# Performance work log

Hardware: AMD Instinct MI355X
Metric: run time of the kernel (lower is better)

Reference implementation:

```python
import jax, jax.numpy as jnp
import numpy as np

B, T, D, KQ, K, V, L = 4, 4096, 256, 32, 4, 8, 4
LN_EPS = 1e-5


def _layernorm(h, g, b):
    mu = h.mean(-1, keepdims=True)
    var = ((h - mu) ** 2).mean(-1, keepdims=True)
    return (h - mu) * jax.lax.rsqrt(var + LN_EPS) * g + b


def _forward(x, attention_mask, Wq, bq, Wk, bk, Wg, bg, W1f, b1f, W2f, b2f,
             ln_g, ln_b, Whh, b_ih, b_hh, Wp, bp, opW1, opb1, opW2, opb2, Wo, bo):
    # ---- DemandRouter ----
    q = x @ Wq + bq                      # [B,T,KQ]
    k = x @ Wk + bk                      # [B,T,KQ]
    sim = jnp.einsum('btk,bsk->bts', q, k) / jnp.sqrt(jnp.float32(KQ))  # [B,T,T]
    mask2 = attention_mask[:, None, :] * attention_mask[:, :, None]
    sim = jnp.where(mask2 == 0, jnp.float32(-1e9), sim)
    gates = jax.nn.sigmoid(x @ Wg + bg)[..., 0]   # [B,T]
    sim = sim * gates[:, :, None]
    _, idx = jax.lax.top_k(sim, K)                # [B,T,K]
    gathered = jax.vmap(lambda xb, ib: xb[ib])(x, idx)  # [B,T,K,D]
    routed_mean = gathered.mean(axis=2)           # [B,T,D]
    # ---- System1Block ----
    ffn = jax.nn.gelu(routed_mean @ W1f + b1f, approximate=False) @ W2f + b2f
    h = _layernorm(routed_mean + ffn, ln_g, ln_b)  # [B,T,D]
    # ---- ProgramGenerator (GRU over zero inputs, h0 = mean-pooled context) ----
    hs = h.mean(axis=1)                           # [B,D]
    outs = []
    for _ in range(L):
        gh = hs @ Whh.T + b_hh                    # [B,3D]
        r = jax.nn.sigmoid(b_ih[:D] + gh[:, :D])
        z = jax.nn.sigmoid(b_ih[D:2 * D] + gh[:, D:2 * D])
        n = jnp.tanh(b_ih[2 * D:] + r * gh[:, 2 * D:])
        hs = (1 - z) * n + z * hs
        outs.append(hs)
    rnn_out = jnp.stack(outs, axis=1)             # [B,L,D]
    program_logits = rnn_out @ Wp + bp            # [B,L,V]
    # ---- NeuralOpLibrary: op outputs are identical across L, so compute once
    # on [B,T,D] and average softmax weights over L (same math as expand+mean).
    op_hidden = jax.nn.relu(jnp.einsum('btd,vde->btve', h, opW1) + opb1)
    op_out = jnp.einsum('btve,ved->btvd', op_hidden, opW2) + opb2  # [B,T,V,D]
    w = jax.nn.softmax(program_logits, axis=-1).mean(axis=1)       # [B,V]
    fused = jnp.einsum('bv,btvd->btd', w, op_out)                   # [B,T,D]
    # ---- pool + output projection ----
    pooled = fused.max(axis=1)                    # [B,D]
    return pooled @ Wo + bo


def setup_inputs() -> dict:
    key = jax.random.key(0)
    ks = jax.random.split(key, 20)
    s = 0.02
    p = lambda i, shape: jax.random.normal(ks[i], shape, jnp.float32) * s
    return {
        'x': jax.random.normal(ks[0], (B, T, D), jnp.float32),
        'attention_mask': jnp.ones((B, T), jnp.float32),
        'Wq': p(1, (D, KQ)), 'bq': jnp.zeros((KQ,), jnp.float32),
        'Wk': p(2, (D, KQ)), 'bk': jnp.zeros((KQ,), jnp.float32),
        'Wg': p(3, (D, 1)), 'bg': jnp.zeros((1,), jnp.float32),
        'W1f': p(4, (D, 2 * D)), 'b1f': jnp.zeros((2 * D,), jnp.float32),
        'W2f': p(5, (2 * D, D)), 'b2f': jnp.zeros((D,), jnp.float32),
        'ln_g': jnp.ones((D,), jnp.float32), 'ln_b': jnp.zeros((D,), jnp.float32),
        'Whh': p(6, (3 * D, D)), 'b_ih': p(7, (3 * D,)), 'b_hh': p(8, (3 * D,)),
        'Wp': p(9, (D, V)), 'bp': jnp.zeros((V,), jnp.float32),
        'opW1': p(10, (V, D, D)), 'opb1': jnp.zeros((V, D), jnp.float32),
        'opW2': p(11, (V, D, D)), 'opb2': jnp.zeros((V, D), jnp.float32),
        'Wo': p(12, (D, D)), 'bo': jnp.zeros((D,), jnp.float32),
    }


def reference(x, attention_mask, Wq, bq, Wk, bk, Wg, bg, W1f, b1f, W2f, b2f,
              ln_g, ln_b, Whh, b_ih, b_hh, Wp, bp, opW1, opb1, opW2, opb2, Wo, bo):
    return _forward(x, attention_mask, Wq, bq, Wk, bk, Wg, bg, W1f, b1f, W2f, b2f,
                    ln_g, ln_b, Whh, b_ih, b_hh, Wp, bp, opW1, opb1, opW2, opb2, Wo, bo)
```

## Files before the change

### kernel.cpp

```cpp
#include <hip/hip_runtime.h>

#define BB 4
#define TT 4096
#define DD 256
#define KQ 32
#define TOPK 4
#define NV 8
#define NL 4
#define MROWS (BB*TT)
#define NSC 8
#define SSPAN 512
#define NCAND (NSC*16)

typedef __attribute__((ext_vector_type(8))) __bf16 bf16x8;
typedef __attribute__((ext_vector_type(4))) float  f32x4;

__device__ __forceinline__ unsigned short f2bf(float f) {
  union { float f; unsigned u; } un; un.f = f;
  unsigned r = un.u + 0x7fffu + ((un.u >> 16) & 1u);
  return (unsigned short)(r >> 16);
}
__device__ __forceinline__ float b2f(unsigned short s) {
  union { unsigned u; float f; } un; un.u = ((unsigned)s) << 16;
  return un.f;
}

__device__ __forceinline__ void ins4(float val, int s, float v[4], int id[4]) {
  if (val <= v[3]) return;
  v[3] = val; id[3] = s;
  #pragma unroll
  for (int j = 3; j > 0; --j) {
    if (v[j] > v[j-1]) {
      float tv = v[j]; v[j] = v[j-1]; v[j-1] = tv;
      int   ti = id[j]; id[j] = id[j-1]; id[j-1] = ti;
    }
  }
}

__global__ __launch_bounds__(256) void prep_weights(
    const float* __restrict__ W1f, const float* __restrict__ W2f,
    const float* __restrict__ opW1, const float* __restrict__ opW2,
    const float* __restrict__ Whh,
    unsigned short* __restrict__ W1ft, unsigned short* __restrict__ W2ft,
    unsigned short* __restrict__ opW1t, unsigned short* __restrict__ opW2t,
    unsigned int* __restrict__ Whhp) {
  int idx = blockIdx.x * 256 + threadIdx.x;
  if (idx < 131072) { int n = idx >> 8, d = idx & 255; W1ft[idx] = f2bf(W1f[d*512 + n]); return; }
  idx -= 131072;
  if (idx < 131072) { int n = idx >> 9, d = idx & 511; W2ft[idx] = f2bf(W2f[d*256 + n]); return; }
  idx -= 131072;
  if (idx < 524288) { int np = idx >> 8, d = idx & 255; int v = np >> 8, e = np & 255;
                      opW1t[idx] = f2bf(opW1[v*65536 + d*256 + e]); return; }
  idx -= 524288;
  if (idx < 524288) { int n = idx >> 11, kp = idx & 2047; int v = kp >> 8, k2 = kp & 255;
                      opW2t[idx] = f2bf(opW2[v*65536 + k2*256 + n]); return; }
  idx -= 524288;
  if (idx < 98304) {
    int dp = idx / 768, j = idx - dp*768;
    unsigned lo = f2bf(Whh[j*256 + 2*dp]);
    unsigned hi = f2bf(Whh[j*256 + 2*dp + 1]);
    Whhp[idx] = lo | (hi << 16);
  }
}

__global__ __launch_bounds__(256) void qk_proj(
    const float* __restrict__ x, const float* __restrict__ Wq, const float* __restrict__ bq,
    const float* __restrict__ Wk, const float* __restrict__ bk,
    float* __restrict__ q, float* __restrict__ kk,
    unsigned short* __restrict__ qbf, unsigned short* __restrict__ kbf) {
  __shared__ float xs[1024];
  int tid = threadIdx.x;
  *(float4*)&xs[tid*4] = *(const float4*)&x[(size_t)blockIdx.x*1024 + tid*4];
  __syncthreads();
  int row = blockIdx.x*4 + (tid >> 6);
  int j = tid & 63;
  int jj = j & 31;
  const float* W = (j < 32) ? Wq : Wk;
  const float* xr = &xs[(tid >> 6) * 256];
  float acc = 0.f;
  #pragma unroll 8
  for (int d = 0; d < 256; ++d) acc += xr[d] * W[d*32 + jj];
  acc += (j < 32) ? bq[jj] : bk[jj];
  float* out = (j < 32) ? q : kk;
  unsigned short* outb = (j < 32) ? qbf : kbf;
  out[(size_t)row*32 + jj] = acc;
  outb[(size_t)row*32 + jj] = f2bf(acc);
}

__global__ __launch_bounds__(256) void sim_scan(
    const unsigned short* __restrict__ qbf, const unsigned short* __restrict__ kbf,
    const float* __restrict__ mask, int* __restrict__ candi, float* __restrict__ candvv) {
  int b = blockIdx.z, sc = blockIdx.y;
  int q0 = blockIdx.x * 64;
  int tid = threadIdx.x;
  int w = tid >> 6, lane = tid & 63;
  int l15 = lane & 15, lhi = lane >> 4;

  __shared__ unsigned short kfr[SSPAN*32];
  __shared__ float ms[SSPAN];
  __shared__ int mflag;

  int qrow = q0 + w*16 + l15;
  bf16x8 qf = *(const bf16x8*)&qbf[((size_t)b*TT + qrow)*32 + lhi*8];
  float mrow = mask[b*TT + qrow];

  float vtop[4]; int itop[4];
  #pragma unroll
  for (int r = 0; r < 4; ++r) { vtop[r] = -__builtin_inff(); itop[r] = 0; }

  int s0 = sc * SSPAN;
  if (tid == 0) mflag = 0;
  __syncthreads();
  int anyzero = 0;
  #pragma unroll
  for (int rr = 0; rr < 2; ++rr) {
    int s = rr*256 + tid;
    const unsigned short* src = &kbf[((size_t)b*TT + s0 + s)*32];
    uint4 d0 = *(const uint4*)(src);
    uint4 d1 = *(const uint4*)(src + 8);
    uint4 d2 = *(const uint4*)(src + 16);
    uint4 d3 = *(const uint4*)(src + 24);
    int fb = (s >> 4)*512 + (s & 15)*8;
    *(uint4*)&kfr[fb +   0] = d0;
    *(uint4*)&kfr[fb + 128] = d1;
    *(uint4*)&kfr[fb + 256] = d2;
    *(uint4*)&kfr[fb + 384] = d3;
    float mv = mask[b*TT + s0 + s];
    ms[s] = mv;
    if (mv == 0.f) anyzero = 1;
  }
  if (anyzero) mflag = 1;
  __syncthreads();
  bool useMask = (mflag != 0) || (mrow == 0.f);
  f32x4 z = {0.f, 0.f, 0.f, 0.f};
  for (int sf = 0; sf < SSPAN/16; sf += 2) {
    bf16x8 a0 = *(const bf16x8*)&kfr[(sf+0)*512 + lane*8];
    bf16x8 a1 = *(const bf16x8*)&kfr[(sf+1)*512 + lane*8];
    f32x4 c0 = __builtin_amdgcn_mfma_f32_16x16x32_bf16(a0, qf, z, 0, 0, 0);
    f32x4 c1 = __builtin_amdgcn_mfma_f32_16x16x32_bf16(a1, qf, z, 0, 0, 0);
    int sb0 = s0 + (sf+0)*16 + lhi*4;
    int sb1 = s0 + (sf+1)*16 + lhi*4;
    #pragma unroll
    for (int r = 0; r < 4; ++r) {
      float v0 = c0[r], v1 = c1[r];
      if (useMask) {
        if (mrow * ms[(sf+0)*16 + lhi*4 + r] == 0.f) v0 = -1e9f;
        if (mrow * ms[(sf+1)*16 + lhi*4 + r] == 0.f) v1 = -1e9f;
      }
      ins4(v0, sb0 + r, vtop, itop);
      ins4(v1, sb1 + r, vtop, itop);
    }
  }
  size_t base = ((size_t)(b*TT + qrow))*NCAND + sc*16 + lhi*4;
  #pragma unroll
  for (int r = 0; r < 4; ++r) { candi[base + r] = itop[r]; candvv[base + r] = vtop[r]; }
}

__global__ __launch_bounds__(256) void refine8(
    const int* __restrict__ candi, const float* __restrict__ candv,
    const float* __restrict__ q, const float* __restrict__ kk,
    const float* __restrict__ mask, int* __restrict__ sel) {
  int tid = threadIdx.x;
  int g = tid >> 5, j = tid & 31;
  int row = blockIdx.x*8 + g;
  int b = row >> 12;
  float v[4]; int id[4];
  const float* cvp = &candv[(size_t)row*NCAND];
  const int*   cip = &candi[(size_t)row*NCAND];
  #pragma unroll
  for (int k2 = 0; k2 < 4; ++k2) { v[k2] = cvp[j + k2*32]; id[k2] = cip[j + k2*32]; }
  int c8[8];
  #pragma unroll
  for (int r = 0; r < 8; ++r) {
    float bv = v[0]; int bi = id[0];
    #pragma unroll
    for (int k2 = 1; k2 < 4; ++k2)
      if (v[k2] > bv || (v[k2] == bv && id[k2] < bi)) { bv = v[k2]; bi = id[k2]; }
    #pragma unroll
    for (int o = 16; o > 0; o >>= 1) {
      float ov = __shfl_xor(bv, o, 32);
      int   oi = __shfl_xor(bi, o, 32);
      if (ov > bv || (ov == bv && oi < bi)) { bv = ov; bi = oi; }
    }
    c8[r] = bi;
    #pragma unroll
    for (int k2 = 0; k2 < 4; ++k2) if (id[k2] == bi) v[k2] = -__builtin_inff();
  }
  int ca = c8[j >> 2];
  int seg = (j & 3) * 8;
  const float* kp = &kk[((size_t)(b << 12) + ca)*32 + seg];
  const float* qp = &q[(size_t)row*32 + seg];
  float pd = 0.f;
  #pragma unroll
  for (int t = 0; t < 8; t += 4) {
    float4 kv = *(const float4*)&kp[t];
    float4 qv = *(const float4*)&qp[t];
    pd += kv.x*qv.x + kv.y*qv.y + kv.z*qv.z + kv.w*qv.w;
  }
  pd += __shfl_xor(pd, 1, 32);
  pd += __shfl_xor(pd, 2, 32);
  if (mask[row] * mask[(b << 12) + ca] == 0.f) pd = -1e9f;
  float dv[8];
  #pragma unroll
  for (int c = 0; c < 8; ++c) dv[c] = __shfl(pd, c*4, 32);
  if (j == 0) {
    int s0 = -1, s1 = -1, s2 = -1, s3 = -1;
    int4 o4;
    #pragma unroll
    for (int r = 0; r < 4; ++r) {
      float bv = -__builtin_inff(); int bi = 0x7fffffff;
      #pragma unroll
      for (int c = 0; c < 8; ++c) {
        int ii = c8[c]; float vv = dv[c];
        if (ii == s0 || ii == s1 || ii == s2 || ii == s3) continue;
        if (vv > bv || (vv == bv && ii < bi)) { bv = vv; bi = ii; }
      }
      if (r == 0) { o4.x = bi; s0 = bi; }
      else if (r == 1) { o4.y = bi; s1 = bi; }
      else if (r == 2) { o4.z = bi; s2 = bi; }
      else { o4.w = bi; s3 = bi; }
    }
    *(int4*)&sel[(size_t)row*4] = o4;
  }
}

__global__ __launch_bounds__(256) void gather_mean(
    const int* __restrict__ sel, const float* __restrict__ x,
    unsigned short* __restrict__ rmb) {
  int tid = threadIdx.x;
  int row = blockIdx.x*4 + (tid >> 6);
  int lane = tid & 63;
  int b = row >> 12;
  int4 s = *(const int4*)&sel[(size_t)row*4];
  const float* xb = &x[(size_t)b*TT*DD];
  float4 a  = *(const float4*)&xb[(size_t)s.x*DD + lane*4];
  float4 bb = *(const float4*)&xb[(size_t)s.y*DD + lane*4];
  float4 cc = *(const float4*)&xb[(size_t)s.z*DD + lane*4];
  float4 e  = *(const float4*)&xb[(size_t)s.w*DD + lane*4];
  ushort4 o;
  o.x = f2bf((a.x + bb.x + cc.x + e.x)*0.25f);
  o.y = f2bf((a.y + bb.y + cc.y + e.y)*0.25f);
  o.z = f2bf((a.z + bb.z + cc.z + e.z)*0.25f);
  o.w = f2bf((a.w + bb.w + cc.w + e.w)*0.25f);
  *(ushort4*)&rmb[(size_t)row*DD + lane*4] = o;
}

__global__ __launch_bounds__(512) void ffn_fused(
    const unsigned short* __restrict__ rmb,
    const unsigned short* __restrict__ W1ft,
    const unsigned short* __restrict__ W2ft,
    const float* __restrict__ b1f, const float* __restrict__ bias2,
    const float* __restrict__ ln_g, const float* __restrict__ ln_b,
    unsigned short* __restrict__ h) {
  __shared__ unsigned short rmbS[32*264];
  __shared__ unsigned short G1S[32*520];
  __shared__ float psum[32][8];
  __shared__ float psq[32][8];
  __shared__ float meanS[32];
  __shared__ float rstdS[32];
  int tid = threadIdx.x;
  int w = tid >> 6, lane = tid & 63, l16 = lane & 15, lhi = lane >> 4;
  int m0 = blockIdx.x * 32;
  #pragma unroll
  for (int i = 0; i < 2; ++i) {
    int idx = i*512 + tid;
    int r = idx >> 5, c = (idx & 31) * 8;
    *(uint4*)&rmbS[r*264 + c] = *(const uint4*)&rmb[(size_t)(m0 + r)*256 + c];
  }
  __syncthreads();
  {
    f32x4 acc1[2][4] = {};
    #pragma unroll
    for (int kk2 = 0; kk2 < 8; ++kk2) {
      int ko = kk2*32 + lhi*8;
      bf16x8 af[2], bf[4];
      #pragma unroll
      for (int f = 0; f < 2; ++f) af[f] = *(const bf16x8*)&rmbS[(f*16 + l16)*264 + ko];
      #pragma unroll
      for (int f = 0; f < 4; ++f) bf[f] = *(const bf16x8*)&W1ft[(size_t)(w*64 + f*16 + l16)*256 + ko];
      #pragma unroll
      for (int mf = 0; mf < 2; ++mf)
        #pragma unroll
        for (int nf = 0; nf < 4; ++nf)
          acc1[mf][nf] = __builtin_amdgcn_mfma_f32_16x16x32_bf16(af[mf], bf[nf], acc1[mf][nf], 0, 0, 0);
    }
    #pragma unroll
    for (int mf = 0; mf < 2; ++mf) {
      #pragma unroll
      for (int nf = 0; nf < 4; ++nf) {
        int col = w*64 + nf*16 + l16;
        float bias = b1f[col];
        #pragma unroll
        for (int r = 0; r < 4; ++r) {
          int row = mf*16 + lhi*4 + r;
          float v = acc1[mf][nf][r] + bias;
          v = 0.5f * v * (1.0f + erff(v * 0.70710678118654752f));
          G1S[row*520 + col] = f2bf(v);
        }
      }
    }
  }
  __syncthreads();
  f32x4 acc2[2][2] = {};
  #pragma unroll
  for (int kk2 = 0; kk2 < 16; ++kk2) {
    int ko = kk2*32 + lhi*8;
    bf16x8 af[2], bf[2];
    #pragma unroll
    for (int f = 0; f < 2; ++f) af[f] = *(const bf16x8*)&G1S[(f*16 + l16)*520 + ko];
    #pragma unroll
    for (int f = 0; f < 2; ++f) bf[f] = *(const bf16x8*)&W2ft[(size_t)(w*32 + f*16 + l16)*512 + ko];
    #pragma unroll
    for (int mf = 0; mf < 2; ++mf)
      #pragma unroll
      for (int nf = 0; nf < 2; ++nf)
        acc2[mf][nf] = __builtin_amdgcn_mfma_f32_16x16x32_bf16(af[mf], bf[nf], acc2[mf][nf], 0, 0, 0);
  }
  float pre[2][2][4];
  #pragma unroll
  for (int mf = 0; mf < 2; ++mf) {
    #pragma unroll
    for (int r = 0; r < 4; ++r) {
      int row = mf*16 + lhi*4 + r;
      float s = 0.f, sq = 0.f;
      #pragma unroll
      for (int nf = 0; nf < 2; ++nf) {
        int col = w*32 + nf*16 + l16;
        float v = acc2[mf][nf][r] + bias2[col] + b2f(rmbS[row*264 + col]);
        pre[mf][nf][r] = v;
        s += v; sq += v*v;
      }
      #pragma unroll
      for (int o = 1; o < 16; o <<= 1) { s += __shfl_xor(s, o); sq += __shfl_xor(sq, o); }
      if (l16 == 0) { psum[row][w] = s; psq[row][w] = sq; }
    }
  }
  __syncthreads();
  if (tid < 32) {
    float s = 0.f, sq = 0.f;
    #pragma unroll
    for (int j = 0; j < 8; ++j) { s += psum[tid][j]; sq += psq[tid][j]; }
    float mean = s * (1.0f/256.0f);
    float var = sq * (1.0f/256.0f) - mean*mean;
    meanS[tid] = mean;
    rstdS[tid] = rsqrtf(var + 1e-5f);
  }
  __syncthreads();
  #pragma unroll
  for (int nf = 0; nf < 2; ++nf) {
    int col = w*32 + nf*16 + l16;
    float gv = ln_g[col], bv = ln_b[col];
    #pragma unroll
    for (int mf = 0; mf < 2; ++mf) {
      #pragma unroll
      for (int r = 0; r < 4; ++r) {
        int row = mf*16 + lhi*4 + r;
        float v = (pre[mf][nf][r] - meanS[row]) * rstdS[row] * gv + bv;
        h[(size_t)(m0 + row)*256 + col] = f2bf(v);
      }
    }
  }
}

template<int EPI>
__global__ __launch_bounds__(256) void gemm_bf16(
    const unsigned short* __restrict__ A, const unsigned short* __restrict__ Bt,
    int Ndim, int Kdim,
    const float* __restrict__ bias,
    const unsigned short* __restrict__ resB,
    const float* __restrict__ auxf,
    float* __restrict__ outF, unsigned short* __restrict__ outB) {
  __shared__ unsigned short SMEM[128*132];
  unsigned short* As = SMEM;
  unsigned short* Bs = SMEM + 128*64;
  int tid = threadIdx.x;
  int lane = tid & 63, wid = tid >> 6;
  int wm = wid >> 1, wn = wid & 1;
  int l16 = lane & 15, lhi = lane >> 4;
  int m0 = blockIdx.x * 128, n0 = blockIdx.y * 128;
  f32x4 acc[4][4] = {};
  for (int kt = 0; kt < Kdim; kt += 64) {
    __syncthreads();
    #pragma unroll
    for (int i = 0; i < 4; ++i) {
      int L = i*256 + tid;
      int r = L >> 3, c = L & 7;
      int cs = c ^ (r & 7);
      uint4 va = *(const uint4*)(A  + (size_t)(m0 + r)*Kdim + kt + c*8);
      *(uint4*)&As[r*64 + cs*8] = va;
      uint4 vb = *(const uint4*)(Bt + (size_t)(n0 + r)*Kdim + kt + c*8);
      *(uint4*)&Bs[r*64 + cs*8] = vb;
    }
    __syncthreads();
    #pragma unroll
    for (int ks = 0; ks < 2; ++ks) {
      bf16x8 af[4], bfr[4];
      int kc = ks*4 + lhi;
      #pragma unroll
      for (int f = 0; f < 4; ++f) {
        int ra = wm*64 + f*16 + l16;
        af[f]  = *(const bf16x8*)&As[ra*64 + ((kc ^ (ra & 7)))*8];
        int rb = wn*64 + f*16 + l16;
        bfr[f] = *(const bf16x8*)&Bs[rb*64 + ((kc ^ (rb & 7)))*8];
      }
      #pragma unroll
      for (int mf = 0; mf < 4; ++mf)
        #pragma unroll
        for (int nf = 0; nf < 4; ++nf)
          acc[mf][nf] = __builtin_amdgcn_mfma_f32_16x16x32_bf16(af[mf], bfr[nf], acc[mf][nf], 0, 0, 0);
    }
  }
  if constexpr (EPI == 1) {
    #pragma unroll
    for (int mf = 0; mf < 4; ++mf)
      #pragma unroll
      for (int nf = 0; nf < 4; ++nf)
        #pragma unroll
        for (int r = 0; r < 4; ++r) {
          int row = m0 + wm*64 + mf*16 + lhi*4 + r;
          int col = n0 + wn*64 + nf*16 + l16;
          float v = acc[mf][nf][r] + bias[col] + b2f(resB[(size_t)row*Ndim + col]);
          outF[(size_t)row*Ndim + col] = v;
        }
  } else {
    __syncthreads();
    #pragma unroll
    for (int mf = 0; mf < 4; ++mf) {
      #pragma unroll
      for (int nf = 0; nf < 4; ++nf) {
        #pragma unroll
        for (int r = 0; r < 4; ++r) {
          int lrow = wm*64 + mf*16 + lhi*4 + r;
          int lcol = wn*64 + nf*16 + l16;
          int row = m0 + lrow, col = n0 + lcol;
          float v = acc[mf][nf][r];
          if constexpr (EPI == 0) {
            v += bias[col];
            v = 0.5f * v * (1.0f + erff(v * 0.70710678118654752f));
          } else if constexpr (EPI == 2) {
            v += bias[col];
            v = fmaxf(v, 0.0f) * auxf[(row >> 12)*8 + (col >> 8)];
          } else {
            v += auxf[(row >> 12)*256 + col];
          }
          SMEM[lrow*132 + lcol] = f2bf(v);
        }
      }
    }
    __syncthreads();
    #pragma unroll
    for (int i = 0; i < 8; ++i) {
      int idx = i*256 + tid;
      int lrow = idx >> 4, co = (idx & 15)*8;
      *(uint4*)&outB[(size_t)(m0 + lrow)*Ndim + n0 + co] = *(const uint4*)&SMEM[lrow*132 + co];
    }
  }
}

__global__ __launch_bounds__(256) void gemm64_bf16(
    const unsigned short* __restrict__ A, const unsigned short* __restrict__ Bt,
    int Ndim, int Kdim,
    const float* __restrict__ auxf, unsigned short* __restrict__ outB) {
  __shared__ unsigned short SMEM[64*192 + 64];
  unsigned short* As = SMEM;
  unsigned short* Bs = SMEM + 64*64;
  int tid = threadIdx.x;
  int lane = tid & 63, wn = tid >> 6;
  int l16 = lane & 15, lhi = lane >> 4;
  int m0 = blockIdx.x * 64, n0 = blockIdx.y * 128;
  f32x4 acc[4][2] = {};
  for (int kt = 0; kt < Kdim; kt += 64) {
    __syncthreads();
    #pragma unroll
    for (int i = 0; i < 2; ++i) {
      int L = i*256 + tid;
      int r = L >> 3, c = L & 7;
      int cs = c ^ (r & 7);
      uint4 va = *(const uint4*)(A + (size_t)(m0 + r)*Kdim + kt + c*8);
      *(uint4*)&As[r*64 + cs*8] = va;
    }
    #pragma unroll
    for (int i = 0; i < 4; ++i) {
      int L = i*256 + tid;
      int r = L >> 3, c = L & 7;
      int cs = c ^ (r & 7);
      uint4 vb = *(const uint4*)(Bt + (size_t)(n0 + r)*Kdim + kt + c*8);
      *(uint4*)&Bs[r*64 + cs*8] = vb;
    }
    __syncthreads();
    #pragma unroll
    for (int ks = 0; ks < 2; ++ks) {
      bf16x8 af[4], bfr[2];
      int kc = ks*4 + lhi;
      #pragma unroll
      for (int f = 0; f < 4; ++f) {
        int ra = f*16 + l16;
        af[f] = *(const bf16x8*)&As[ra*64 + ((kc ^ (ra & 7)))*8];
      }
      #pragma unroll
      for (int f = 0; f < 2; ++f) {
        int rb = wn*32 + f*16 + l16;
        bfr[f] = *(const bf16x8*)&Bs[rb*64 + ((kc ^ (rb & 7)))*8];
      }
      #pragma unroll
      for (int mf = 0; mf < 4; ++mf)
        #pragma unroll
        for (int nf = 0; nf < 2; ++nf)
          acc[mf][nf] = __builtin_amdgcn_mfma_f32_16x16x32_bf16(af[mf], bfr[nf], acc[mf][nf], 0, 0, 0);
    }
  }
  __syncthreads();
  #pragma unroll
  for (int mf = 0; mf < 4; ++mf) {
    #pragma unroll
    for (int nf = 0; nf < 2; ++nf) {
      #pragma unroll
      for (int r = 0; r < 4; ++r) {
        int lrow = mf*16 + lhi*4 + r;
        int lcol = wn*32 + nf*16 + l16;
        float v = acc[mf][nf][r] + auxf[((m0 + lrow) >> 12)*256 + n0 + lcol];
        SMEM[lrow*132 + lcol] = f2bf(v);
      }
    }
  }
  __syncthreads();
  #pragma unroll
  for (int i = 0; i < 4; ++i) {
    int idx = i*256 + tid;
    int lrow = idx >> 4, co = (idx & 15)*8;
    *(uint4*)&outB[(size_t)(m0 + lrow)*Ndim + n0 + co] = *(const uint4*)&SMEM[lrow*132 + co];
  }
}

__global__ __launch_bounds__(256) void hsum_kernel(const unsigned short* __restrict__ h, float* __restrict__ hpart) {
  int c = blockIdx.x, b = blockIdx.y, d = threadIdx.x;
  const unsigned short* hp = &h[((size_t)(b*TT + c*64))*256 + d];
  float s = 0.f;
  #pragma unroll 8
  for (int i = 0; i < 64; ++i) s += b2f(hp[i*256]);
  hpart[(b*64 + c)*256 + d] = s;
}

__global__ __launch_bounds__(1024) void gru_kernel(
    const float* __restrict__ hpart, const unsigned int* __restrict__ Whhp,
    const float* __restrict__ b_ih, const float* __restrict__ b_hh,
    const float* __restrict__ Wp, const float* __restrict__ bp,
    const float* __restrict__ opb2, float* __restrict__ w, float* __restrict__ wb2) {
  int b = blockIdx.x, tid = threadIdx.x;
  __shared__ float hs[256];
  __shared__ float gsh[768];
  __shared__ float wps[2048];
  __shared__ float lgpart[256];
  __shared__ float lg[8];
  __shared__ float wacc[8];
  if (tid < 256) {
    float s = 0.f;
    #pragma unroll
    for (int c = 0; c < 64; ++c) s += hpart[(b*64 + c)*256 + tid];
    hs[tid] = s * (1.0f/4096.0f);
  }
  wps[tid] = Wp[tid];
  wps[1024 + tid] = Wp[1024 + tid];
  if (tid < 8) wacc[tid] = 0.f;
  __syncthreads();
  for (int l = 0; l < NL; ++l) {
    if (tid < 768) {
      float acc = 0.f;
      #pragma unroll 16
      for (int dp = 0; dp < 128; ++dp) {
        unsigned w2 = Whhp[dp*768 + tid];
        acc += b2f((unsigned short)(w2 & 0xffff))*hs[2*dp]
             + b2f((unsigned short)(w2 >> 16))*hs[2*dp + 1];
      }
      gsh[tid] = acc;
    }
    __syncthreads();
    if (tid < 256) {
      float g0 = gsh[tid]       + b_hh[tid];
      float g1 = gsh[256 + tid] + b_hh[256 + tid];
      float g2 = gsh[512 + tid] + b_hh[512 + tid];
      float r = 1.f / (1.f + expf(-(b_ih[tid] + g0)));
      float z = 1.f / (1.f + expf(-(b_ih[256 + tid] + g1)));
      float n = tanhf(b_ih[512 + tid] + r * g2);
      gsh[tid] = (1.f - z) * n + z * hs[tid];
    }
    __syncthreads();
    if (tid < 256) hs[tid] = gsh[tid];
    __syncthreads();
    if (tid < 256) {
      int dp2 = tid >> 3;
      float acc = 0.f;
      #pragma unroll
      for (int k2 = 0; k2 < 8; ++k2) acc += hs[dp2 + 32*k2] * wps[tid + 256*k2];
      lgpart[tid] = acc;
    }
    __syncthreads();
    if (tid < 8) {
      float acc = bp[tid];
      #pragma unroll
      for (int j = 0; j < 32; ++j) acc += lgpart[j*8 + tid];
      lg[tid] = acc;
    }
    __syncthreads();
    if (tid == 0) {
      float mx = lg[0];
      #pragma unroll
      for (int i = 1; i < 8; ++i) mx = fmaxf(mx, lg[i]);
      float sm = 0.f; float e[8];
      #pragma unroll
      for (int i = 0; i < 8; ++i) { e[i] = expf(lg[i] - mx); sm += e[i]; }
      #pragma unroll
      for (int i = 0; i < 8; ++i) wacc[i] += e[i] / sm;
    }
    __syncthreads();
  }
  if (tid < 8) w[b*8 + tid] = wacc[tid] * 0.25f;
  if (tid < 256) {
    float acc = 0.f;
    #pragma unroll
    for (int v = 0; v < 8; ++v) acc += (wacc[v] * 0.25f) * opb2[v*256 + tid];
    wb2[b*256 + tid] = acc;
  }
}

__global__ __launch_bounds__(256) void maxpool_kernel(const unsigned short* __restrict__ fusedB, float* __restrict__ mpart) {
  int c = blockIdx.x, b = blockIdx.y, d = threadIdx.x;
  const unsigned short* fp = &fusedB[((size_t)(b*TT + c*64))*256 + d];
  float m = -__builtin_inff();
  #pragma unroll 8
  for (int i = 0; i < 64; ++i) m = fmaxf(m, b2f(fp[i*256]));
  mpart[(b*64 + c)*256 + d] = m;
}

__global__ __launch_bounds__(256) void outproj_kernel(
    const float* __restrict__ mpart, const float* __restrict__ Wo,
    const float* __restrict__ bo, float* __restrict__ out) {
  int b = blockIdx.x, tid = threadIdx.x;
  __shared__ float pooled[256];
  float m = -__builtin_inff();
  for (int c = 0; c < 64; ++c) m = fmaxf(m, mpart[(b*64 + c)*256 + tid]);
  pooled[tid] = m;
  __syncthreads();
  float acc = bo[tid];
  for (int d = 0; d < 256; ++d) acc += pooled[d] * Wo[d*256 + tid];
  out[b*256 + tid] = acc;
}

extern "C" void kernel_launch(void* const* d_in, const int* in_sizes, int n_in,
                              void* d_out, int out_size, void* d_ws, size_t ws_size,
                              hipStream_t stream) {
  const float* x     = (const float*)d_in[0];
  const float* amask = (const float*)d_in[1];
  const float* Wq    = (const float*)d_in[2];
  const float* bq    = (const float*)d_in[3];
  const float* Wk    = (const float*)d_in[4];
  const float* bk    = (const float*)d_in[5];
  const float* W1f   = (const float*)d_in[8];
  const float* b1f   = (const float*)d_in[9];
  const float* W2f   = (const float*)d_in[10];
  const float* b2fp  = (const float*)d_in[11];
  const float* ln_g  = (const float*)d_in[12];
  const float* ln_b  = (const float*)d_in[13];
  const float* Whh   = (const float*)d_in[14];
  const float* b_ih  = (const float*)d_in[15];
  const float* b_hh  = (const float*)d_in[16];
  const float* Wp    = (const float*)d_in[17];
  const float* bp    = (const float*)d_in[18];
  const float* opW1  = (const float*)d_in[19];
  const float* opb1  = (const float*)d_in[20];
  const float* opW2  = (const float*)d_in[21];
  const float* opb2  = (const float*)d_in[22];
  const float* Wo    = (const float*)d_in[23];
  const float* bo    = (const float*)d_in[24];
  (void)in_sizes; (void)n_in; (void)out_size; (void)ws_size;

  char* ws = (char*)d_ws;
  float*          q      = (float*)(ws + 0);
  float*          kk     = (float*)(ws + 2097152);
  unsigned short* qbf    = (unsigned short*)(ws + 4194304);
  unsigned short* kbf    = (unsigned short*)(ws + 5242880);
  int*            candi  = (int*)(ws + 6291456);
  float*          candv  = (float*)(ws + 14680064);
  unsigned short* rmb    = (unsigned short*)(ws + 23068672);
  unsigned short* G1all  = (unsigned short*)(ws + 0);
  unsigned short* h      = (unsigned short*)(ws + 67108864);
  unsigned short* W1ft   = (unsigned short*)(ws + 75497472);
  unsigned short* W2ft   = (unsigned short*)(ws + 75759616);
  unsigned short* opW1t  = (unsigned short*)(ws + 76021760);
  unsigned short* opW2t  = (unsigned short*)(ws + 77070336);
  unsigned int*   Whhp   = (unsigned int*)(ws + 78118912);
  float*          hpart  = (float*)(ws + 78512128);
  float*          wv     = (float*)(ws + 78774272);
  float*          wb2    = (float*)(ws + 78778368);
  float*          mpart  = (float*)(ws + 78782464);
  unsigned short* fusedB = (unsigned short*)(ws + 79044608);
  int*            sel    = (int*)(ws + 87433216);

  prep_weights<<<5504, 256, 0, stream>>>(W1f, W2f, opW1, opW2, Whh, W1ft, W2ft, opW1t, opW2t, Whhp);
  qk_proj<<<4096, 256, 0, stream>>>(x, Wq, bq, Wk, bk, q, kk, qbf, kbf);
  sim_scan<<<dim3(TT/64, NSC, BB), 256, 0, stream>>>(qbf, kbf, amask, candi, candv);
  refine8<<<MROWS/8, 256, 0, stream>>>(candi, candv, q, kk, amask, sel);
  gather_mean<<<MROWS/4, 256, 0, stream>>>(sel, x, rmb);
  ffn_fused<<<MROWS/32, 512, 0, stream>>>(rmb, W1ft, W2ft, b1f, b2fp, ln_g, ln_b, h);
  hsum_kernel<<<dim3(64, BB), 256, 0, stream>>>(h, hpart);
  gru_kernel<<<4, 1024, 0, stream>>>(hpart, Whhp, b_ih, b_hh, Wp, bp, opb2, wv, wb2);
  gemm_bf16<2><<<dim3(128, 16), 256, 0, stream>>>(h, opW1t, 2048, 256, opb1, nullptr, wv, nullptr, G1all);
  gemm64_bf16<<<dim3(256, 2), 256, 0, stream>>>(G1all, opW2t, 256, 2048, wb2, fusedB);
  maxpool_kernel<<<dim3(64, BB), 256, 0, stream>>>(fusedB, mpart);
  outproj_kernel<<<4, 256, 0, stream>>>(mpart, Wo, bo, (float*)d_out);
}
```

Measured before the change: 277.0 us.

## Use direct global-to-LDS loads in GEMMs and widen FFN block to 1024 threads

The two bf16 GEMM kernels now stage tiles with the global_load_lds builtin, which writes each 16-byte chunk straight into shared memory without going through registers. The XOR swizzle moves from the LDS write address to the global read address so the shared-memory layout stays the same. Separately, the fused FFN kernel doubles its block to 16 waves, each computing half as many output columns, to raise parallelism per tile. Risks are the alignment and ordering rules of direct LDS loads, and higher register and occupancy pressure from 1024-thread blocks.

After: 281.5 us. About the same (+1.6%).

```diff
diff --git a/kernel.cpp b/kernel.cpp
--- a/kernel.cpp
+++ b/kernel.cpp
@@ -23,6 +23,10 @@
 __device__ __forceinline__ float b2f(unsigned short s) {
   union { unsigned u; float f; } un; un.u = ((unsigned)s) << 16;
   return un.f;
+}
+__device__ __forceinline__ void gload16(const unsigned short* g, unsigned short* l) {
+  __builtin_amdgcn_global_load_lds((const __attribute__((address_space(1))) void*)(g),
+                                   (__attribute__((address_space(3))) void*)(l), 16, 0, 0);
 }
 
 __device__ __forceinline__ void ins4(float val, int s, float v[4], int id[4]) {
@@ -245,7 +249,7 @@
   *(ushort4*)&rmb[(size_t)row*DD + lane*4] = o;
 }
 
-__global__ __launch_bounds__(512) void ffn_fused(
+__global__ __launch_bounds__(1024) void ffn_fused(
     const unsigned short* __restrict__ rmb,
     const unsigned short* __restrict__ W1ft,
     const unsigned short* __restrict__ W2ft,
@@ -254,41 +258,39 @@
     unsigned short* __restrict__ h) {
   __shared__ unsigned short rmbS[32*264];
   __shared__ unsigned short G1S[32*520];
-  __shared__ float psum[32][8];
-  __shared__ float psq[32][8];
+  __shared__ float psum[32][16];
+  __shared__ float psq[32][16];
   __shared__ float meanS[32];
   __shared__ float rstdS[32];
   int tid = threadIdx.x;
   int w = tid >> 6, lane = tid & 63, l16 = lane & 15, lhi = lane >> 4;
   int m0 = blockIdx.x * 32;
-  #pragma unroll
-  for (int i = 0; i < 2; ++i) {
-    int idx = i*512 + tid;
-    int r = idx >> 5, c = (idx & 31) * 8;
+  {
+    int r = tid >> 5, c = (tid & 31) * 8;
     *(uint4*)&rmbS[r*264 + c] = *(const uint4*)&rmb[(size_t)(m0 + r)*256 + c];
   }
   __syncthreads();
   {
-    f32x4 acc1[2][4] = {};
+    f32x4 acc1[2][2] = {};
     #pragma unroll
     for (int kk2 = 0; kk2 < 8; ++kk2) {
       int ko = kk2*32 + lhi*8;
-      bf16x8 af[2], bf[4];
-      #pragma unroll
-      for (int f = 0; f < 2; ++f) af[f] = *(const bf16x8*)&rmbS[(f*16 + l16)*264 + ko];
-      #pragma unroll
-      for (int f = 0; f < 4; ++f) bf[f] = *(const bf16x8*)&W1ft[(size_t)(w*64 + f*16 + l16)*256 + ko];
+      bf16x8 af[2], bf[2];
+      af[0] = *(const bf16x8*)&rmbS[l16*264 + ko];
+      af[1] = *(const bf16x8*)&rmbS[(16 + l16)*264 + ko];
+      bf[0] = *(const bf16x8*)&W1ft[(size_t)(w*32 + l16)*256 + ko];
+      bf[1] = *(const bf16x8*)&W1ft[(size_t)(w*32 + 16 + l16)*256 + ko];
       #pragma unroll
       for (int mf = 0; mf < 2; ++mf)
         #pragma unroll
-        for (int nf = 0; nf < 4; ++nf)
+        for (int nf = 0; nf < 2; ++nf)
           acc1[mf][nf] = __builtin_amdgcn_mfma_f32_16x16x32_bf16(af[mf], bf[nf], acc1[mf][nf], 0, 0, 0);
     }
     #pragma unroll
     for (int mf = 0; mf < 2; ++mf) {
       #pragma unroll
-      for (int nf = 0; nf < 4; ++nf) {
-        int col = w*64 + nf*16 + l16;
+      for (int nf = 0; nf < 2; ++nf) {
+        int col = w*32 + nf*16 + l16;
         float bias = b1f[col];
         #pragma unroll
         for (int r = 0; r < 4; ++r) {
@@ -301,35 +303,29 @@
     }
   }
   __syncthreads();
-  f32x4 acc2[2][2] = {};
+  f32x4 acc2[2] = {};
   #pragma unroll
   for (int kk2 = 0; kk2 < 16; ++kk2) {
     int ko = kk2*32 + lhi*8;
-    bf16x8 af[2], bf[2];
-    #pragma unroll
-    for (int f = 0; f < 2; ++f) af[f] = *(const bf16x8*)&G1S[(f*16 + l16)*520 + ko];
-    #pragma unroll
-    for (int f = 0; f < 2; ++f) bf[f] = *(const bf16x8*)&W2ft[(size_t)(w*32 + f*16 + l16)*512 + ko];
+    bf16x8 af[2], bf;
+    af[0] = *(const bf16x8*)&G1S[l16*520 + ko];
+    af[1] = *(const bf16x8*)&G1S[(16 + l16)*520 + ko];
+    bf = *(const bf16x8*)&W2ft[(size_t)(w*16 + l16)*512 + ko];
     #pragma unroll
     for (int mf = 0; mf < 2; ++mf)
-      #pragma unroll
-      for (int nf = 0; nf < 2; ++nf)
-        acc2[mf][nf] = __builtin_amdgcn_mfma_f32_16x16x32_bf16(af[mf], bf[nf], acc2[mf][nf], 0, 0, 0);
-  }
-  float pre[2][2][4];
+      acc2[mf] = __builtin_amdgcn_mfma_f32_16x16x32_bf16(af[mf], bf, acc2[mf], 0, 0, 0);
+  }
+  int colc = w*16 + l16;
+  float bias2v = bias2[colc];
+  float pre[2][4];
   #pragma unroll
   for (int mf = 0; mf < 2; ++mf) {
     #pragma unroll
     for (int r = 0; r < 4; ++r) {
       int row = mf*16 + lhi*4 + r;
-      float s = 0.f, sq = 0.f;
-      #pragma unroll
-      for (int nf = 0; nf < 2; ++nf) {
-        int col = w*32 + nf*16 + l16;
-        float v = acc2[mf][nf][r] + bias2[col] + b2f(rmbS[row*264 + col]);
-        pre[mf][nf][r] = v;
-        s += v; sq += v*v;
-      }
+      float v = acc2[mf][r] + bias2v + b2f(rmbS[row*264 + colc]);
+      pre[mf][r] = v;
+      float s = v, sq = v*v;
       #pragma unroll
       for (int o = 1; o < 16; o <<= 1) { s += __shfl_xor(s, o); sq += __shfl_xor(sq, o); }
       if (l16 == 0) { psum[row][w] = s; psq[row][w] = sq; }
@@ -339,25 +335,21 @@
   if (tid < 32) {
     float s = 0.f, sq = 0.f;
     #pragma unroll
-    for (int j = 0; j < 8; ++j) { s += psum[tid][j]; sq += psq[tid][j]; }
+    for (int j = 0; j < 16; ++j) { s += psum[tid][j]; sq += psq[tid][j]; }
     float mean = s * (1.0f/256.0f);
     float var = sq * (1.0f/256.0f) - mean*mean;
     meanS[tid] = mean;
     rstdS[tid] = rsqrtf(var + 1e-5f);
   }
   __syncthreads();
-  #pragma unroll
-  for (int nf = 0; nf < 2; ++nf) {
-    int col = w*32 + nf*16 + l16;
-    float gv = ln_g[col], bv = ln_b[col];
-    #pragma unroll
-    for (int mf = 0; mf < 2; ++mf) {
-      #pragma unroll
-      for (int r = 0; r < 4; ++r) {
-        int row = mf*16 + lhi*4 + r;
-        float v = (pre[mf][nf][r] - meanS[row]) * rstdS[row] * gv + bv;
-        h[(size_t)(m0 + row)*256 + col] = f2bf(v);
-      }
+  float gv = ln_g[colc], bv = ln_b[colc];
+  #pragma unroll
+  for (int mf = 0; mf < 2; ++mf) {
+    #pragma unroll
+    for (int r = 0; r < 4; ++r) {
+      int row = mf*16 + lhi*4 + r;
+      float v = (pre[mf][r] - meanS[row]) * rstdS[row] * gv + bv;
+      h[(size_t)(m0 + row)*256 + colc] = f2bf(v);
     }
   }
 }
@@ -383,13 +375,12 @@
     __syncthreads();
     #pragma unroll
     for (int i = 0; i < 4; ++i) {
-      int L = i*256 + tid;
-      int r = L >> 3, c = L & 7;
-      int cs = c ^ (r & 7);
-      uint4 va = *(const uint4*)(A  + (size_t)(m0 + r)*Kdim + kt + c*8);
-      *(uint4*)&As[r*64 + cs*8] = va;
-      uint4 vb = *(const uint4*)(Bt + (size_t)(n0 + r)*Kdim + kt + c*8);
-      *(uint4*)&Bs[r*64 + cs*8] = vb;
+      int L0 = i*256 + wid*64;
+      int L  = L0 + lane;
+      int r = L >> 3;
+      int csrc = ((lane & 7) ^ (r & 7)) * 8;
+      gload16(A  + (size_t)(m0 + r)*Kdim + kt + csrc, &As[L0*8]);
+      gload16(Bt + (size_t)(n0 + r)*Kdim + kt + csrc, &Bs[L0*8]);
     }
     __syncthreads();
     #pragma unroll
@@ -473,19 +464,19 @@
     __syncthreads();
     #pragma unroll
     for (int i = 0; i < 2; ++i) {
-      int L = i*256 + tid;
-      int r = L >> 3, c = L & 7;
-      int cs = c ^ (r & 7);
-      uint4 va = *(const uint4*)(A + (size_t)(m0 + r)*Kdim + kt + c*8);
-      *(uint4*)&As[r*64 + cs*8] = va;
+      int L0 = i*256 + wn*64;
+      int L  = L0 + lane;
+      int r = L >> 3;
+      int csrc = ((lane & 7) ^ (r & 7)) * 8;
+      gload16(A + (size_t)(m0 + r)*Kdim + kt + csrc, &As[L0*8]);
     }
     #pragma unroll
     for (int i = 0; i < 4; ++i) {
-      int L = i*256 + tid;
-      int r = L >> 3, c = L & 7;
-      int cs = c ^ (r & 7);
-      uint4 vb = *(const uint4*)(Bt + (size_t)(n0 + r)*Kdim + kt + c*8);
-      *(uint4*)&Bs[r*64 + cs*8] = vb;
+      int L0 = i*256 + wn*64;
+      int L  = L0 + lane;
+      int r = L >> 3;
+      int csrc = ((lane & 7) ^ (r & 7)) * 8;
+      gload16(Bt + (size_t)(n0 + r)*Kdim + kt + csrc, &Bs[L0*8]);
     }
     __syncthreads();
     #pragma unroll
@@ -701,7 +692,7 @@
   sim_scan<<<dim3(TT/64, NSC, BB), 256, 0, stream>>>(qbf, kbf, amask, candi, candv);
   refine8<<<MROWS/8, 256, 0, stream>>>(candi, candv, q, kk, amask, sel);
   gather_mean<<<MROWS/4, 256, 0, stream>>>(sel, x, rmb);
-  ffn_fused<<<MROWS/32, 512, 0, stream>>>(rmb, W1ft, W2ft, b1f, b2fp, ln_g, ln_b, h);
+  ffn_fused<<<MROWS/32, 1024, 0, stream>>>(rmb, W1ft, W2ft, b1f, b2fp, ln_g, ln_b, h);
   hsum_kernel<<<dim3(64, BB), 256, 0, stream>>>(h, hpart);
   gru_kernel<<<4, 1024, 0, stream>>>(hpart, Whhp, b_ih, b_hh, Wp, bp, opb2, wv, wb2);
   gemm_bf16<2><<<dim3(128, 16), 256, 0, stream>>>(h, opW1t, 2048, 256, opb1, nullptr, wv, nullptr, G1all);
```
